# Performance work log

Hardware: AMD Instinct MI355X
Metric: run time of the kernel (lower is better)

The kernel has to match this reference:

```python
import jax, jax.numpy as jnp
import numpy as np
import math

T, N, F, A, NH = 2048, 64, 64, 64, 8
QG, QH, DG, DH = 256, 256, 256, 256
HORIZON = 16


def setup_inputs() -> dict:
    key = jax.random.key(0)
    ks = jax.random.split(key, 12)
    s = 0.05  # xavier-ish scale
    return {
        "x_fix": jax.random.normal(ks[0], (T, F), jnp.float32),
        "x_att": jax.random.normal(ks[1], (T, N, A), jnp.float32),
        "train_horizon": HORIZON,
        # query GRUCell: input = fix + 2*A*NH
        "q_gru_w_ih": jax.random.normal(ks[2], (3 * QG, F + 2 * A * NH), jnp.float32) * s,
        "q_gru_w_hh": jax.random.normal(ks[3], (3 * QG, QG), jnp.float32) * s,
        "q_gru_b_ih": jnp.zeros((3 * QG,), jnp.float32),
        "q_gru_b_hh": jnp.zeros((3 * QG,), jnp.float32),
        # q_hidden: input = QG + F + A*NH
        "q_hid_w": jax.random.normal(ks[4], (QH, QG + F + A * NH), jnp.float32) * s,
        "q_hid_b": jnp.zeros((QH,), jnp.float32),
        "weight_q": jax.random.normal(ks[5], (QH, A * NH), jnp.float32) * s,
        # decoder GRU: input = F + A*NH
        "dec_gru_w_ih": jax.random.normal(ks[6], (3 * DG, F + A * NH), jnp.float32) * s,
        "dec_gru_w_hh": jax.random.normal(ks[7], (3 * DG, DG), jnp.float32) * s,
        "dec_gru_b_ih": jnp.zeros((3 * DG,), jnp.float32),
        "dec_gru_b_hh": jnp.zeros((3 * DG,), jnp.float32),
        # dec_hidden: input = DG + F + A*NH + A
        "dec_hid_w": jax.random.normal(ks[8], (DH, DG + F + A * NH + A), jnp.float32) * s,
        "dec_hid_b": jnp.zeros((DH,), jnp.float32),
        "dec_out_w": jax.random.normal(ks[9], (A, DH), jnp.float32) * s,
        "dec_out_b": jnp.zeros((A,), jnp.float32),
    }


def _gru_cell(x, h, w_ih, w_hh, b_ih, b_hh):
    """PyTorch GRUCell math (gate order r,z,n)."""
    gi = w_ih @ x + b_ih
    gh = w_hh @ h + b_hh
    ir, iz, in_ = jnp.split(gi, 3)
    hr, hz, hn = jnp.split(gh, 3)
    r = jax.nn.sigmoid(ir + hr)
    z = jax.nn.sigmoid(iz + hz)
    n = jnp.tanh(in_ + r * hn)
    return (1.0 - z) * n + z * h


def reference(x_fix, x_att, train_horizon,
              q_gru_w_ih, q_gru_w_hh, q_gru_b_ih, q_gru_b_hh,
              q_hid_w, q_hid_b, weight_q,
              dec_gru_w_ih, dec_gru_w_hh, dec_gru_b_ih, dec_gru_b_hh,
              dec_hid_w, dec_hid_b, dec_out_w, dec_out_b):
    t, n_obj, a = x_att.shape
    nh_a = weight_q.shape[1]
    nh = nh_a // a
    scale = 1.0 / math.sqrt(a)

    # ---- recurrent query generation (sequential over time) ----
    def step(carry, inp):
        h, query = carry
        fix_t, att_t = inp                                   # [F], [N, A]
        attw = jax.nn.softmax((query.reshape(nh, a) @ att_t.T) * scale, axis=1)  # [NH, N]
        att_v = (attw @ att_t).reshape(-1)                   # [NH*A]
        h2 = _gru_cell(jnp.concatenate([fix_t, att_v, query]), h,
                       q_gru_w_ih, q_gru_w_hh, q_gru_b_ih, q_gru_b_hh)
        hid = jax.nn.relu(q_hid_w @ jnp.concatenate([h2, fix_t, att_v]) + q_hid_b)
        query2 = hid @ weight_q
        return (h2, query2), (attw, att_v)

    h0 = jnp.zeros((q_gru_w_hh.shape[1],), x_fix.dtype)
    q0 = jnp.ones((nh_a,), x_fix.dtype)
    (q_gru_n, query_n), (attw, att_a) = jax.lax.scan(step, (h0, q0), (x_fix, x_att))

    # ---- decoder (training path; dropout_p=0, noise_std=0 -> identity) ----
    hz = train_horizon
    # replicate-pad attw back hz steps in time, drop last hz: dec_attw[t] = attw[max(t-hz,0)]
    dec_attw = jnp.concatenate(
        [jnp.broadcast_to(attw[:1], (hz,) + attw.shape[1:]), attw[:-hz]], axis=0)  # [T, NH, N]
    dec_att_a = jnp.einsum('thn,tnd->thd', dec_attw, x_att).reshape(t, -1)          # [T, NH*A]
    dec_x = jnp.concatenate([x_fix, dec_att_a], axis=-1)                            # [T, F+NH*A]

    def dec_step(hd, xt):
        hd2 = _gru_cell(xt, hd, dec_gru_w_ih, dec_gru_w_hh, dec_gru_b_ih, dec_gru_b_hh)
        return hd2, hd2

    dg0 = jnp.zeros((dec_gru_w_hh.shape[1],), x_fix.dtype)
    dec_gru_n, dec_gru_a = jax.lax.scan(dec_step, dg0, dec_x)                       # [T, DG]

    feat = jnp.concatenate([dec_gru_a, dec_x], axis=-1)                             # [T, DG+F+NH*A]
    feat_b = jnp.broadcast_to(feat[:, None, :], (t, n_obj, feat.shape[-1]))
    inp = jnp.concatenate([feat_b, x_att], axis=-1)                                 # [T, N, DG+F+NH*A+A]
    hid = jax.nn.relu(inp @ dec_hid_w.T + dec_hid_b)
    pred = jax.nn.relu(hid @ dec_out_w.T + dec_out_b)                               # [T, N, A]

    return pred, attw, q_gru_n, dec_gru_n, query_n
```

## Files before the change

kernel.cpp:

```cpp
#include <hip/hip_runtime.h>
#include <math.h>

#define TT 2048
#define HZ 16
#define NBLK 32
#define NTH 512

#define OUT_ATTW   (2048*64*64)
#define OUT_QGRU   (OUT_ATTW + 2048*8*64)
#define OUT_DECGRU (OUT_QGRU + 256)
#define OUT_QN     (OUT_DECGRU + 256)

#define WSO_MB1    0
#define WSO_QACC   8192
#define WSO_QCNT   14336
#define WSO_ZEND   14464
#define WSO_GIFIX  14464
#define WSO_HIDFIX (WSO_GIFIX + 2048*768*4)
#define WSO_W2T    (WSO_HIDFIX + 2048*256*4)
#define WSO_DAVA   (WSO_W2T + 256*64*4)
#define WSO_DECH   (WSO_DAVA + 2048*512*4)
#define WSO_FEAT   (WSO_DECH + 2048*256*4)
#define WSO_SBUF   (WSO_FEAT + 2048*832*4)

__device__ __forceinline__ float warp_sum(float v) {
#pragma unroll
  for (int o = 32; o > 0; o >>= 1) v += __shfl_down(v, o, 64);
  return v;
}
__device__ __forceinline__ float warp_max(float v) {
#pragma unroll
  for (int o = 32; o > 0; o >>= 1) v = fmaxf(v, __shfl_down(v, o, 64));
  return v;
}
__device__ __forceinline__ float sigf(float x) { return 1.f / (1.f + __expf(-x)); }
__device__ __forceinline__ float dot4(float4 a, float4 b) {
  return a.x*b.x + a.y*b.y + a.z*b.z + a.w*b.w;
}
__device__ __forceinline__ unsigned long long aload64(const unsigned long long* p) {
  return __hip_atomic_load(p, __ATOMIC_RELAXED, __HIP_MEMORY_SCOPE_AGENT);
}
__device__ __forceinline__ void astore64(unsigned long long* p, unsigned long long v) {
  __hip_atomic_store(p, v, __ATOMIC_RELAXED, __HIP_MEMORY_SCOPE_AGENT);
}
__device__ __forceinline__ unsigned long long mbpack(float f, unsigned tag) {
  return ((unsigned long long)tag << 32) | (unsigned long long)__float_as_uint(f);
}
__device__ __forceinline__ float mbpoll(const unsigned long long* p, unsigned tag) {
  unsigned long long v = aload64(p);
  while ((unsigned)(v >> 32) != tag) {
    __builtin_amdgcn_s_sleep(1);
    v = aload64(p);
  }
  return __uint_as_float((unsigned)v);
}

__global__ void transpose_k(const float* __restrict__ w2,
                            float* __restrict__ w2T) {
  int e = blockIdx.x * 256 + threadIdx.x;
  int r = e >> 6, a = e & 63;
  w2T[e] = w2[a * 256 + r];
}

__global__ void __launch_bounds__(256) gemm64(
    const float* __restrict__ X, int ldx,
    const float* __restrict__ W, int ldw, int woff,
    const float* __restrict__ bias,
    float* __restrict__ C, int crows, int K) {
  __shared__ float Xs[64 * 65];
  __shared__ float Ws[64 * 65];
  int t0 = blockIdx.x * 64, r0 = blockIdx.y * 64;
  int tid = threadIdx.x;
  int u = tid & 15, v = tid >> 4;
  float acc[4][4];
#pragma unroll
  for (int i = 0; i < 4; i++)
#pragma unroll
    for (int j = 0; j < 4; j++) acc[i][j] = 0.f;

  for (int kc = 0; kc < K; kc += 64) {
    for (int idx = tid; idx < 4096; idx += 256) {
      int row = idx >> 6, col = idx & 63;
      Xs[row * 65 + col] = X[(size_t)(t0 + row) * ldx + kc + col];
      Ws[row * 65 + col] = W[(size_t)(r0 + row) * ldw + woff + kc + col];
    }
    __syncthreads();
#pragma unroll 8
    for (int k = 0; k < 64; k++) {
      float xs[4], ws[4];
#pragma unroll
      for (int i = 0; i < 4; i++) xs[i] = Xs[(v + 16 * i) * 65 + k];
#pragma unroll
      for (int j = 0; j < 4; j++) ws[j] = Ws[(u + 16 * j) * 65 + k];
#pragma unroll
      for (int i = 0; i < 4; i++)
#pragma unroll
        for (int j = 0; j < 4; j++) acc[i][j] += xs[i] * ws[j];
    }
    __syncthreads();
  }
#pragma unroll
  for (int i = 0; i < 4; i++)
#pragma unroll
    for (int j = 0; j < 4; j++) {
      int t = t0 + v + 16 * i, r = r0 + u + 16 * j;
      C[(size_t)t * crows + r] = acc[i][j] + bias[r];
    }
}

__global__ void __launch_bounds__(512) seq_kernel(
    const float* __restrict__ x_fix,
    const float* __restrict__ x_att,
    const float* __restrict__ w_ih,
    const float* __restrict__ w_hh,
    const float* __restrict__ b_hh,
    const float* __restrict__ q_hid_w,
    const float* __restrict__ wq,
    const float* __restrict__ dwih,
    const float* __restrict__ dwhh,
    const float* __restrict__ dbih,
    const float* __restrict__ dbhh,
    const float* __restrict__ gi_fix,
    const float* __restrict__ hid_fix,
    unsigned long long* __restrict__ mb1,
    float* __restrict__ qacc,
    unsigned* __restrict__ qcnt,
    float* __restrict__ dava,
    float* __restrict__ dec_hist,
    float* __restrict__ out) {
  __shared__ float att_s[64 * 65];
  __shared__ float ring_s[16][512];
  __shared__ __align__(16) float avq_s[1024];
  __shared__ float qk_s[512];
  __shared__ __align__(16) float xcat_s[576];
  __shared__ __align__(16) float hid8_s[8];
  __shared__ __align__(16) float h_s[256];
  __shared__ __align__(16) float dech_s[256];
  __shared__ float g_s[4][8];
  __shared__ float dg_s[4][8];

  const int tid = threadIdx.x;
  const int bid = blockIdx.x;
  const int lane = tid & 63, wv = tid >> 6;

  for (int i = tid; i < 1024; i += NTH) avq_s[i] = (i >= 512) ? 1.f : 0.f;
  if (tid < 256) { h_s[tid] = 0.f; dech_s[tid] = 0.f; }
  {
    const float4* g4 = (const float4*)x_att;
    float4 a = g4[tid * 2], b = g4[tid * 2 + 1];
    int row = tid >> 3, c0 = (tid & 7) * 8;
    float* d = &att_s[row * 65 + c0];
    d[0]=a.x; d[1]=a.y; d[2]=a.z; d[3]=a.w; d[4]=b.x; d[5]=b.y; d[6]=b.z; d[7]=b.w;
  }
  if (tid < 64) xcat_s[tid] = x_fix[tid];
  __syncthreads();

  for (int t = 0; t <= TT; ++t) {
    if (t > 0) {
      {
        float f = mbpoll(mb1 + (size_t)((t - 1) & 1) * 512 + tid, (unsigned)t);
        int b = tid >> 4, j = tid & 15;
        if (j < 8) h_s[b * 8 + j] = f;
        else dech_s[b * 8 + j - 8] = f;
        if (t >= 2 && tid < 16)
          __hip_atomic_store(&qacc[(size_t)((t - 1) % 3) * 512 + bid * 16 + tid],
                             0.f, __ATOMIC_RELAXED, __HIP_MEMORY_SCOPE_AGENT);
      }
      __syncthreads();
      {
        int row = bid * 8 + wv;
        const float4* W = (const float4*)(q_hid_w + (size_t)row * 832);
        float acc = dot4(W[lane], ((const float4*)h_s)[lane]);
        acc += dot4(W[80 + lane], ((const float4*)avq_s)[lane]);
        acc += dot4(W[144 + lane], ((const float4*)avq_s)[64 + lane]);
        float s = warp_sum(acc);
        if (lane == 0)
          hid8_s[wv] = fmaxf(s + hid_fix[(size_t)(t - 1) * 256 + row], 0.f);
      }
      __syncthreads();
      {
        float hv[8];
#pragma unroll
        for (int r = 0; r < 8; r++) hv[r] = hid8_s[r];
        float partial = 0.f;
#pragma unroll
        for (int r = 0; r < 8; r++)
          partial += hv[r] * wq[(size_t)(bid * 8 + r) * 512 + tid];
        __hip_atomic_fetch_add(&qacc[(size_t)(t % 3) * 512 + tid], partial,
                               __ATOMIC_RELAXED, __HIP_MEMORY_SCOPE_AGENT);
        asm volatile("s_waitcnt vmcnt(0)" ::: "memory");
      }
      __syncthreads();
      if (tid == 0) {
        __hip_atomic_fetch_add(qcnt, 1u, __ATOMIC_RELAXED,
                               __HIP_MEMORY_SCOPE_AGENT);
        unsigned target = 32u * (unsigned)t;
        while (__hip_atomic_load(qcnt, __ATOMIC_RELAXED,
                                 __HIP_MEMORY_SCOPE_AGENT) < target)
          __builtin_amdgcn_s_sleep(1);
      }
      __syncthreads();
      {
        float qv = __hip_atomic_load(&qacc[(size_t)(t % 3) * 512 + tid],
                                     __ATOMIC_RELAXED, __HIP_MEMORY_SCOPE_AGENT);
        avq_s[512 + tid] = qv;
        if (t == TT) {
          if (bid == 0) {
            if (tid < 256) {
              out[OUT_QGRU + tid] = h_s[tid];
              out[OUT_DECGRU + tid] = dech_s[tid];
            }
            out[OUT_QN + tid] = qv;
          }
          break;
        }
      }
      __syncthreads();
    }

    float4 pfa, pfb;
    {
      int tn = (t + 1 < TT) ? t + 1 : t;
      const float4* g4 = (const float4*)(x_att + (size_t)tn * 4096);
      pfa = g4[tid * 2];
      pfb = g4[tid * 2 + 1];
    }
    {
      float acc = 0.f;
#pragma unroll 16
      for (int a = 0; a < 64; a++)
        acc += avq_s[512 + wv * 64 + a] * att_s[lane * 65 + a];
      acc *= 0.125f;
      float m = __shfl(warp_max(acc), 0, 64);
      float e = __expf(acc - m);
      float s = __shfl(warp_sum(e), 0, 64);
      qk_s[wv * 64 + lane] = e / s;
    }
    {
      const float* rg = (t == 0) ? &qk_s[0] : ring_s[(t >= 16) ? (t & 15) : 0];
      float av = 0.f, dv = 0.f;
#pragma unroll 8
      for (int n = 0; n < 64; n++) {
        float xv = att_s[n * 65 + lane];
        av += qk_s[wv * 64 + n] * xv;
        dv += rg[wv * 64 + n] * xv;
      }
      avq_s[wv * 64 + lane] = av;
      xcat_s[64 + wv * 64 + lane] = dv;
    }
    __syncthreads();
    {
      float accg[3], acch[3];
      int rows[3];
#pragma unroll
      for (int k = 0; k < 3; k++) {
        int m = wv * 3 + k;
        rows[k] = ((m >> 3) * 256) + bid * 8 + (m & 7);
        accg[k] = 0.f; acch[k] = 0.f;
      }
      const float4* in4 = (const float4*)avq_s;
#pragma unroll
      for (int c0 = 0; c0 < 4; c0++) {
        int c = lane + 64 * c0;
        float4 v = in4[c];
#pragma unroll
        for (int k = 0; k < 3; k++) {
          const float4* W = (const float4*)(w_ih + (size_t)rows[k] * 1088 + 64);
          accg[k] += dot4(W[c], v);
        }
      }
      {
        const float4* h4 = (const float4*)h_s;
        float4 vh = h4[lane];
#pragma unroll
        for (int k = 0; k < 3; k++) {
          const float4* Wh = (const float4*)(w_hh + (size_t)rows[k] * 256);
          acch[k] += dot4(Wh[lane], vh);
        }
      }
#pragma unroll
      for (int k = 0; k < 3; k++) {
        int m = wv * 3 + k;
        int gate = m >> 3, idx = m & 7;
        if (gate < 2) {
          float s = warp_sum(accg[k] + acch[k]);
          if (lane == 0)
            g_s[gate][idx] = s + gi_fix[(size_t)t * 768 + rows[k]] + b_hh[rows[k]];
        } else {
          float sg = warp_sum(accg[k]);
          float sh = warp_sum(acch[k]);
          if (lane == 0) {
            g_s[2][idx] = sg + gi_fix[(size_t)t * 768 + rows[k]];
            g_s[3][idx] = sh + b_hh[rows[k]];
          }
        }
      }
    }
    {
      float accg[3], acch[3];
      int rows[3];
#pragma unroll
      for (int k = 0; k < 3; k++) {
        int m = wv * 3 + k;
        rows[k] = ((m >> 3) * 256) + bid * 8 + (m & 7);
        accg[k] = 0.f; acch[k] = 0.f;
      }
      const float4* x4 = (const float4*)xcat_s;
#pragma unroll
      for (int c0 = 0; c0 < 3; c0++) {
        int c = lane + 64 * c0;
        if (c < 144) {
          float4 v = x4[c];
#pragma unroll
          for (int k = 0; k < 3; k++) {
            const float4* W = (const float4*)(dwih + (size_t)rows[k] * 576);
            accg[k] += dot4(W[c], v);
          }
        }
      }
      {
        const float4* dh4 = (const float4*)dech_s;
        float4 vh = dh4[lane];
#pragma unroll
        for (int k = 0; k < 3; k++) {
          const float4* Wh = (const float4*)(dwhh + (size_t)rows[k] * 256);
          acch[k] += dot4(Wh[lane], vh);
        }
      }
#pragma unroll
      for (int k = 0; k < 3; k++) {
        int m = wv * 3 + k;
        int gate = m >> 3, idx = m & 7;
        if (gate < 2) {
          float s = warp_sum(accg[k] + acch[k]);
          if (lane == 0)
            dg_s[gate][idx] = s + dbih[rows[k]] + dbhh[rows[k]];
        } else {
          float sg = warp_sum(accg[k]);
          float sh = warp_sum(acch[k]);
          if (lane == 0) {
            dg_s[2][idx] = sg + dbih[rows[k]];
            dg_s[3][idx] = sh + dbhh[rows[k]];
          }
        }
      }
    }
    __syncthreads();
    if (tid < 8) {
      float r = sigf(g_s[0][tid]), z = sigf(g_s[1][tid]);
      float nn = tanhf(g_s[2][tid] + r * g_s[3][tid]);
      float h2 = (1.f - z) * nn + z * h_s[bid * 8 + tid];
      astore64(&mb1[(size_t)(t & 1) * 512 + bid * 16 + tid],
               mbpack(h2, (unsigned)(t + 1)));
    } else if (tid < 16) {
      int i = tid - 8;
      float r = sigf(dg_s[0][i]), z = sigf(dg_s[1][i]);
      float nn = tanhf(dg_s[2][i] + r * dg_s[3][i]);
      float d2 = (1.f - z) * nn + z * dech_s[bid * 8 + i];
      astore64(&mb1[(size_t)(t & 1) * 512 + bid * 16 + tid],
               mbpack(d2, (unsigned)(t + 1)));
      dec_hist[(size_t)t * 256 + bid * 8 + i] = d2;
    }
    if (tid < 16) {
      out[OUT_ATTW + (size_t)t * 512 + bid * 16 + tid] = qk_s[bid * 16 + tid];
      dava[(size_t)t * 512 + bid * 16 + tid] = xcat_s[64 + bid * 16 + tid];
    }
    ring_s[t & 15][tid] = qk_s[tid];
    {
      int row = tid >> 3, c0 = (tid & 7) * 8;
      float* d = &att_s[row * 65 + c0];
      d[0]=pfa.x; d[1]=pfa.y; d[2]=pfa.z; d[3]=pfa.w;
      d[4]=pfb.x; d[5]=pfb.y; d[6]=pfb.z; d[7]=pfb.w;
    }
    if (tid >= 448) {
      int i = tid - 448;
      int tn = (t + 1 < TT) ? t + 1 : t;
      xcat_s[i] = x_fix[tn * 64 + i];
    }
  }
}

__global__ void featcopy(const float* __restrict__ dec_hist,
                         const float* __restrict__ x_fix,
                         const float* __restrict__ dava,
                         float* __restrict__ feat) {
  int t = blockIdx.x, tid = threadIdx.x;
  float* f = feat + (size_t)t * 832;
  f[tid] = dec_hist[(size_t)t * 256 + tid];
  if (tid < 64) f[256 + tid] = x_fix[t * 64 + tid];
  for (int i = tid; i < 512; i += 256) f[320 + i] = dava[(size_t)t * 512 + i];
}

__global__ void __launch_bounds__(256) final_k(
    const float* __restrict__ x_att,
    const float* __restrict__ s,
    const float* __restrict__ w1,
    const float* __restrict__ w2T,
    const float* __restrict__ b2,
    float* __restrict__ pred) {
  __shared__ float att_s[4096];
  __shared__ float s_s[256];
  __shared__ float hid_s[32 * 256];
  int t = blockIdx.x, tid = threadIdx.x, lane = tid & 63, wv = tid >> 6;
  for (int i = tid; i < 4096; i += 256) att_s[i] = x_att[(size_t)t * 4096 + i];
  s_s[tid] = s[(size_t)t * 256 + tid];
  float4 w1v[16];
  const float4* W1a4 = (const float4*)(w1 + (size_t)tid * 896 + 832);
#pragma unroll
  for (int q = 0; q < 16; q++) w1v[q] = W1a4[q];
  float bb = b2[lane];
  __syncthreads();
  for (int ch = 0; ch < 2; ch++) {
    for (int nl = 0; nl < 32; nl++) {
      int n = ch * 32 + nl;
      const float4* a4 = (const float4*)(att_s + n * 64);
      float acc = s_s[tid];
#pragma unroll
      for (int q = 0; q < 16; q++) acc += dot4(w1v[q], a4[q]);
      hid_s[nl * 256 + tid] = fmaxf(acc, 0.f);
    }
    __syncthreads();
    float accb[8];
#pragma unroll
    for (int j = 0; j < 8; j++) accb[j] = bb;
    for (int r = 0; r < 256; r++) {
      float w = w2T[r * 64 + lane];
#pragma unroll
      for (int j = 0; j < 8; j++) accb[j] += w * hid_s[(wv * 8 + j) * 256 + r];
    }
#pragma unroll
    for (int j = 0; j < 8; j++) {
      int n = ch * 32 + wv * 8 + j;
      pred[(size_t)t * 4096 + n * 64 + lane] = fmaxf(accb[j], 0.f);
    }
    __syncthreads();
  }
}

extern "C" void kernel_launch(void* const* d_in, const int* in_sizes, int n_in,
                              void* d_out, int out_size, void* d_ws, size_t ws_size,
                              hipStream_t stream) {
  const float* x_fix = (const float*)d_in[0];
  const float* x_att = (const float*)d_in[1];
  const float* qwih = (const float*)d_in[3];
  const float* qwhh = (const float*)d_in[4];
  const float* qbih = (const float*)d_in[5];
  const float* qbhh = (const float*)d_in[6];
  const float* qhw = (const float*)d_in[7];
  const float* qhb = (const float*)d_in[8];
  const float* wq = (const float*)d_in[9];
  const float* dwih = (const float*)d_in[10];
  const float* dwhh = (const float*)d_in[11];
  const float* dbih = (const float*)d_in[12];
  const float* dbhh = (const float*)d_in[13];
  const float* w1 = (const float*)d_in[14];
  const float* b1 = (const float*)d_in[15];
  const float* w2 = (const float*)d_in[16];
  const float* b2 = (const float*)d_in[17];
  float* out = (float*)d_out;

  char* ws = (char*)d_ws;
  unsigned long long* mb1 = (unsigned long long*)(ws + WSO_MB1);
  float* qacc = (float*)(ws + WSO_QACC);
  unsigned* qcnt = (unsigned*)(ws + WSO_QCNT);
  float* gi_fix = (float*)(ws + WSO_GIFIX);
  float* hid_fix = (float*)(ws + WSO_HIDFIX);
  float* w2T = (float*)(ws + WSO_W2T);
  float* dava = (float*)(ws + WSO_DAVA);
  float* dec_hist = (float*)(ws + WSO_DECH);
  float* feat = (float*)(ws + WSO_FEAT);
  float* sbuf = (float*)(ws + WSO_SBUF);

  hipMemsetAsync(ws, 0, WSO_ZEND, stream);

  transpose_k<<<64, 256, 0, stream>>>(w2, w2T);
  gemm64<<<dim3(32, 12), 256, 0, stream>>>(x_fix, 64, qwih, 1088, 0, qbih,
                                           gi_fix, 768, 64);
  gemm64<<<dim3(32, 4), 256, 0, stream>>>(x_fix, 64, qhw, 832, 256, qhb,
                                          hid_fix, 256, 64);

  seq_kernel<<<NBLK, NTH, 0, stream>>>(x_fix, x_att, qwih, qwhh, qbhh,
                                       qhw, wq, dwih, dwhh, dbih, dbhh,
                                       gi_fix, hid_fix, mb1, qacc, qcnt,
                                       dava, dec_hist, out);

  featcopy<<<2048, 256, 0, stream>>>(dec_hist, x_fix, dava, feat);
  gemm64<<<dim3(32, 4), 256, 0, stream>>>(feat, 832, w1, 896, 0, b1,
                                          sbuf, 256, 832);
  final_k<<<2048, 256, 0, stream>>>(x_att, sbuf, w1, w2T, b2, out);
}
```

Measured before the change: 22.72 ms.

## Restructure sequential loop with fixed-point atomic reductions and counter-tagged completion polling

Reorganises the per-timestep cross-block schedule of the persistent recurrent kernel. The q_hidden projection becomes a scatter-reduce over a transposed weight, using fixed-point 64-bit atomics whose top byte counts contributions, so consumers poll for completion instead of sharing a global counter barrier. The hidden-state matvecs and the decoder GRU input are moved after the mailbox exchange so they overlap with waiting, and ring-buffer slots are cleared for reuse. The aim is fewer grid-wide synchronisation round trips per step, at the cost of fixed-point precision loss and more complex slot-recycling logic.

```diff
diff --git a/kernel.cpp b/kernel.cpp
--- a/kernel.cpp
+++ b/kernel.cpp
@@ -2,7 +2,6 @@
 #include <math.h>
 
 #define TT 2048
-#define HZ 16
 #define NBLK 32
 #define NTH 512
 
@@ -12,16 +11,19 @@
 #define OUT_QN     (OUT_DECGRU + 256)
 
 #define WSO_MB1    0
-#define WSO_QACC   8192
-#define WSO_QCNT   14336
-#define WSO_ZEND   14464
-#define WSO_GIFIX  14464
+#define WSO_HIDACC 8192
+#define WSO_QACC   16384
+#define WSO_ZEND   32768
+#define WSO_GIFIX  32768
 #define WSO_HIDFIX (WSO_GIFIX + 2048*768*4)
-#define WSO_W2T    (WSO_HIDFIX + 2048*256*4)
+#define WSO_QHWT   (WSO_HIDFIX + 2048*256*4)
+#define WSO_W2T    (WSO_QHWT + 832*256*4)
 #define WSO_DAVA   (WSO_W2T + 256*64*4)
 #define WSO_DECH   (WSO_DAVA + 2048*512*4)
 #define WSO_FEAT   (WSO_DECH + 2048*256*4)
 #define WSO_SBUF   (WSO_FEAT + 2048*832*4)
+
+#define PAYMASK ((1ULL<<56)-1)
 
 __device__ __forceinline__ float warp_sum(float v) {
 #pragma unroll
@@ -54,12 +56,41 @@
   }
   return __uint_as_float((unsigned)v);
 }
-
-__global__ void transpose_k(const float* __restrict__ w2,
+__device__ __forceinline__ unsigned long long rpack(float v) {
+  long long f = (long long)((double)v * 268435456.0);
+  return (1ULL << 56) + (unsigned long long)(f + (1LL << 41));
+}
+__device__ __forceinline__ float runpack(unsigned long long u) {
+  long long S = (long long)(u & PAYMASK) - (32LL << 41);
+  return (float)((double)S * 3.725290298461914e-09);
+}
+__device__ __forceinline__ unsigned long long cpoll(unsigned long long* p) {
+  unsigned long long u = aload64(p);
+  while ((u >> 56) != 32ULL) {
+    __builtin_amdgcn_s_sleep(1);
+    u = aload64(p);
+  }
+  return u;
+}
+__device__ __forceinline__ void radd(unsigned long long* p, float v) {
+  __hip_atomic_fetch_add(p, rpack(v), __ATOMIC_RELAXED, __HIP_MEMORY_SCOPE_AGENT);
+}
+
+__global__ void transpose_k(const float* __restrict__ qhw,
+                            const float* __restrict__ w2,
+                            float* __restrict__ qhwT,
                             float* __restrict__ w2T) {
-  int e = blockIdx.x * 256 + threadIdx.x;
-  int r = e >> 6, a = e & 63;
-  w2T[e] = w2[a * 256 + r];
+  int g = blockIdx.x * 256 + threadIdx.x;
+  if (g < 832 * 256) {
+    int c = g >> 8, r = g & 255;
+    qhwT[g] = qhw[r * 832 + c];
+  } else {
+    int e = g - 832 * 256;
+    if (e < 16384) {
+      int r = e >> 6, a = e & 63;
+      w2T[e] = w2[a * 256 + r];
+    }
+  }
 }
 
 __global__ void __launch_bounds__(256) gemm64(
@@ -114,7 +145,7 @@
     const float* __restrict__ w_ih,
     const float* __restrict__ w_hh,
     const float* __restrict__ b_hh,
-    const float* __restrict__ q_hid_w,
+    const float* __restrict__ qhwT,
     const float* __restrict__ wq,
     const float* __restrict__ dwih,
     const float* __restrict__ dwhh,
@@ -123,8 +154,8 @@
     const float* __restrict__ gi_fix,
     const float* __restrict__ hid_fix,
     unsigned long long* __restrict__ mb1,
-    float* __restrict__ qacc,
-    unsigned* __restrict__ qcnt,
+    unsigned long long* __restrict__ hidacc,
+    unsigned long long* __restrict__ qacc,
     float* __restrict__ dava,
     float* __restrict__ dec_hist,
     float* __restrict__ out) {
@@ -133,7 +164,8 @@
   __shared__ __align__(16) float avq_s[1024];
   __shared__ float qk_s[512];
   __shared__ __align__(16) float xcat_s[576];
-  __shared__ __align__(16) float hid8_s[8];
+  __shared__ float hidown_s[8];
+  __shared__ float h2own_s[8];
   __shared__ __align__(16) float h_s[256];
   __shared__ __align__(16) float dech_s[256];
   __shared__ float g_s[4][8];
@@ -142,6 +174,14 @@
   const int tid = threadIdx.x;
   const int bid = blockIdx.x;
   const int lane = tid & 63, wv = tid >> 6;
+
+  int qrows[3];
+#pragma unroll
+  for (int k = 0; k < 3; k++) {
+    int m = wv * 3 + k;
+    qrows[k] = ((m >> 3) * 256) + bid * 8 + (m & 7);
+  }
+  float acch_q[3] = {0.f, 0.f, 0.f};
 
   for (int i = tid; i < 1024; i += NTH) avq_s[i] = (i >= 512) ? 1.f : 0.f;
   if (tid < 256) { h_s[tid] = 0.f; dech_s[tid] = 0.f; }
@@ -155,75 +195,17 @@
   if (tid < 64) xcat_s[tid] = x_fix[tid];
   __syncthreads();
 
-  for (int t = 0; t <= TT; ++t) {
-    if (t > 0) {
-      {
-        float f = mbpoll(mb1 + (size_t)((t - 1) & 1) * 512 + tid, (unsigned)t);
-        int b = tid >> 4, j = tid & 15;
-        if (j < 8) h_s[b * 8 + j] = f;
-        else dech_s[b * 8 + j - 8] = f;
-        if (t >= 2 && tid < 16)
-          __hip_atomic_store(&qacc[(size_t)((t - 1) % 3) * 512 + bid * 16 + tid],
-                             0.f, __ATOMIC_RELAXED, __HIP_MEMORY_SCOPE_AGENT);
-      }
-      __syncthreads();
-      {
-        int row = bid * 8 + wv;
-        const float4* W = (const float4*)(q_hid_w + (size_t)row * 832);
-        float acc = dot4(W[lane], ((const float4*)h_s)[lane]);
-        acc += dot4(W[80 + lane], ((const float4*)avq_s)[lane]);
-        acc += dot4(W[144 + lane], ((const float4*)avq_s)[64 + lane]);
-        float s = warp_sum(acc);
-        if (lane == 0)
-          hid8_s[wv] = fmaxf(s + hid_fix[(size_t)(t - 1) * 256 + row], 0.f);
-      }
-      __syncthreads();
-      {
-        float hv[8];
-#pragma unroll
-        for (int r = 0; r < 8; r++) hv[r] = hid8_s[r];
-        float partial = 0.f;
-#pragma unroll
-        for (int r = 0; r < 8; r++)
-          partial += hv[r] * wq[(size_t)(bid * 8 + r) * 512 + tid];
-        __hip_atomic_fetch_add(&qacc[(size_t)(t % 3) * 512 + tid], partial,
-                               __ATOMIC_RELAXED, __HIP_MEMORY_SCOPE_AGENT);
-        asm volatile("s_waitcnt vmcnt(0)" ::: "memory");
-      }
-      __syncthreads();
-      if (tid == 0) {
-        __hip_atomic_fetch_add(qcnt, 1u, __ATOMIC_RELAXED,
-                               __HIP_MEMORY_SCOPE_AGENT);
-        unsigned target = 32u * (unsigned)t;
-        while (__hip_atomic_load(qcnt, __ATOMIC_RELAXED,
-                                 __HIP_MEMORY_SCOPE_AGENT) < target)
-          __builtin_amdgcn_s_sleep(1);
-      }
-      __syncthreads();
-      {
-        float qv = __hip_atomic_load(&qacc[(size_t)(t % 3) * 512 + tid],
-                                     __ATOMIC_RELAXED, __HIP_MEMORY_SCOPE_AGENT);
-        avq_s[512 + tid] = qv;
-        if (t == TT) {
-          if (bid == 0) {
-            if (tid < 256) {
-              out[OUT_QGRU + tid] = h_s[tid];
-              out[OUT_DECGRU + tid] = dech_s[tid];
-            }
-            out[OUT_QN + tid] = qv;
-          }
-          break;
-        }
-      }
-      __syncthreads();
-    }
-
+  for (int t = 0; t < TT; ++t) {
+    const int HB = t & 3;
+    const int QB = (t + 1) & 3;
     float4 pfa, pfb;
+    float fixpf = 0.f;
     {
       int tn = (t + 1 < TT) ? t + 1 : t;
       const float4* g4 = (const float4*)(x_att + (size_t)tn * 4096);
       pfa = g4[tid * 2];
       pfb = g4[tid * 2 + 1];
+      if (tid >= 448) fixpf = x_fix[tn * 64 + (tid - 448)];
     }
     {
       float acc = 0.f;
@@ -236,28 +218,17 @@
       float s = __shfl(warp_sum(e), 0, 64);
       qk_s[wv * 64 + lane] = e / s;
     }
-    {
-      const float* rg = (t == 0) ? &qk_s[0] : ring_s[(t >= 16) ? (t & 15) : 0];
-      float av = 0.f, dv = 0.f;
+    __syncthreads();
+    {
+      float av = 0.f;
 #pragma unroll 8
-      for (int n = 0; n < 64; n++) {
-        float xv = att_s[n * 65 + lane];
-        av += qk_s[wv * 64 + n] * xv;
-        dv += rg[wv * 64 + n] * xv;
-      }
+      for (int n = 0; n < 64; n++) av += qk_s[wv * 64 + n] * att_s[n * 65 + lane];
       avq_s[wv * 64 + lane] = av;
-      xcat_s[64 + wv * 64 + lane] = dv;
-    }
-    __syncthreads();
-    {
-      float accg[3], acch[3];
-      int rows[3];
-#pragma unroll
-      for (int k = 0; k < 3; k++) {
-        int m = wv * 3 + k;
-        rows[k] = ((m >> 3) * 256) + bid * 8 + (m & 7);
-        accg[k] = 0.f; acch[k] = 0.f;
-      }
+      if (t == 0) xcat_s[64 + wv * 64 + lane] = av;
+    }
+    __syncthreads();
+    {
+      float accg[3] = {0.f, 0.f, 0.f};
       const float4* in4 = (const float4*)avq_s;
 #pragma unroll
       for (int c0 = 0; c0 < 4; c0++) {
@@ -265,17 +236,8 @@
         float4 v = in4[c];
 #pragma unroll
         for (int k = 0; k < 3; k++) {
-          const float4* W = (const float4*)(w_ih + (size_t)rows[k] * 1088 + 64);
+          const float4* W = (const float4*)(w_ih + (size_t)qrows[k] * 1088 + 64);
           accg[k] += dot4(W[c], v);
-        }
-      }
-      {
-        const float4* h4 = (const float4*)h_s;
-        float4 vh = h4[lane];
-#pragma unroll
-        for (int k = 0; k < 3; k++) {
-          const float4* Wh = (const float4*)(w_hh + (size_t)rows[k] * 256);
-          acch[k] += dot4(Wh[lane], vh);
         }
       }
 #pragma unroll
@@ -283,28 +245,21 @@
         int m = wv * 3 + k;
         int gate = m >> 3, idx = m & 7;
         if (gate < 2) {
-          float s = warp_sum(accg[k] + acch[k]);
+          float s = warp_sum(accg[k] + acch_q[k]);
           if (lane == 0)
-            g_s[gate][idx] = s + gi_fix[(size_t)t * 768 + rows[k]] + b_hh[rows[k]];
+            g_s[gate][idx] = s + gi_fix[(size_t)t * 768 + qrows[k]] + b_hh[qrows[k]];
         } else {
           float sg = warp_sum(accg[k]);
-          float sh = warp_sum(acch[k]);
+          float sh = warp_sum(acch_q[k]);
           if (lane == 0) {
-            g_s[2][idx] = sg + gi_fix[(size_t)t * 768 + rows[k]];
-            g_s[3][idx] = sh + b_hh[rows[k]];
+            g_s[2][idx] = sg + gi_fix[(size_t)t * 768 + qrows[k]];
+            g_s[3][idx] = sh + b_hh[qrows[k]];
           }
         }
       }
     }
-    {
-      float accg[3], acch[3];
-      int rows[3];
-#pragma unroll
-      for (int k = 0; k < 3; k++) {
-        int m = wv * 3 + k;
-        rows[k] = ((m >> 3) * 256) + bid * 8 + (m & 7);
-        accg[k] = 0.f; acch[k] = 0.f;
-      }
+    if (t == 0) {
+      float accg[3] = {0.f, 0.f, 0.f};
       const float4* x4 = (const float4*)xcat_s;
 #pragma unroll
       for (int c0 = 0; c0 < 3; c0++) {
@@ -313,18 +268,9 @@
           float4 v = x4[c];
 #pragma unroll
           for (int k = 0; k < 3; k++) {
-            const float4* W = (const float4*)(dwih + (size_t)rows[k] * 576);
+            const float4* W = (const float4*)(dwih + (size_t)qrows[k] * 576);
             accg[k] += dot4(W[c], v);
           }
-        }
-      }
-      {
-        const float4* dh4 = (const float4*)dech_s;
-        float4 vh = dh4[lane];
-#pragma unroll
-        for (int k = 0; k < 3; k++) {
-          const float4* Wh = (const float4*)(dwhh + (size_t)rows[k] * 256);
-          acch[k] += dot4(Wh[lane], vh);
         }
       }
 #pragma unroll
@@ -332,15 +278,13 @@
         int m = wv * 3 + k;
         int gate = m >> 3, idx = m & 7;
         if (gate < 2) {
-          float s = warp_sum(accg[k] + acch[k]);
-          if (lane == 0)
-            dg_s[gate][idx] = s + dbih[rows[k]] + dbhh[rows[k]];
+          float s = warp_sum(accg[k]);
+          if (lane == 0) dg_s[gate][idx] = s + dbih[qrows[k]] + dbhh[qrows[k]];
         } else {
           float sg = warp_sum(accg[k]);
-          float sh = warp_sum(acch[k]);
           if (lane == 0) {
-            dg_s[2][idx] = sg + dbih[rows[k]];
-            dg_s[3][idx] = sh + dbhh[rows[k]];
+            dg_s[2][idx] = sg + dbih[qrows[k]];
+            dg_s[3][idx] = dbhh[qrows[k]];
           }
         }
       }
@@ -350,6 +294,7 @@
       float r = sigf(g_s[0][tid]), z = sigf(g_s[1][tid]);
       float nn = tanhf(g_s[2][tid] + r * g_s[3][tid]);
       float h2 = (1.f - z) * nn + z * h_s[bid * 8 + tid];
+      h2own_s[tid] = h2;
       astore64(&mb1[(size_t)(t & 1) * 512 + bid * 16 + tid],
                mbpack(h2, (unsigned)(t + 1)));
     } else if (tid < 16) {
@@ -360,10 +305,12 @@
       astore64(&mb1[(size_t)(t & 1) * 512 + bid * 16 + tid],
                mbpack(d2, (unsigned)(t + 1)));
       dec_hist[(size_t)t * 256 + bid * 8 + i] = d2;
-    }
-    if (tid < 16) {
-      out[OUT_ATTW + (size_t)t * 512 + bid * 16 + tid] = qk_s[bid * 16 + tid];
-      dava[(size_t)t * 512 + bid * 16 + tid] = xcat_s[64 + bid * 16 + tid];
+    } else if (tid < 32) {
+      int i = tid - 16;
+      out[OUT_ATTW + (size_t)t * 512 + bid * 16 + i] = qk_s[bid * 16 + i];
+    } else if (tid < 48) {
+      int i = tid - 32;
+      dava[(size_t)t * 512 + bid * 16 + i] = xcat_s[64 + bid * 16 + i];
     }
     ring_s[t & 15][tid] = qk_s[tid];
     {
@@ -372,11 +319,118 @@
       d[0]=pfa.x; d[1]=pfa.y; d[2]=pfa.z; d[3]=pfa.w;
       d[4]=pfb.x; d[5]=pfb.y; d[6]=pfb.z; d[7]=pfb.w;
     }
-    if (tid >= 448) {
-      int i = tid - 448;
-      int tn = (t + 1 < TT) ? t + 1 : t;
-      xcat_s[i] = x_fix[tn * 64 + i];
-    }
+    __syncthreads();
+    if (tid < 256) {
+      float c = 0.f;
+      const float* Wh = qhwT + (size_t)(bid * 8) * 256 + tid;
+#pragma unroll
+      for (int k = 0; k < 8; k++) c += Wh[k * 256] * h2own_s[k];
+      const float* Wa = qhwT + (size_t)(320 + bid * 16) * 256 + tid;
+#pragma unroll
+      for (int k = 0; k < 16; k++) c += Wa[k * 256] * avq_s[bid * 16 + k];
+      radd(&hidacc[(size_t)HB * 256 + tid], c);
+    }
+    if (t >= 1) astore64(&qacc[(size_t)((t - 1) & 3) * 512 + tid], 0ULL);
+    if (tid < 8) {
+      unsigned long long* slot = &hidacc[(size_t)HB * 256 + bid * 8 + tid];
+      unsigned long long u = cpoll(slot);
+      astore64(slot, 0ULL);
+      hidown_s[tid] =
+          fmaxf(runpack(u) + hid_fix[(size_t)t * 256 + bid * 8 + tid], 0.f);
+    } else {
+      int jj = tid - 8;
+      int slot_t1 = (t + 1 >= 16) ? ((t + 1) & 15) : 0;
+      const float* rg = ring_s[slot_t1];
+      {
+        int h = jj >> 6, a = jj & 63;
+        float dv = 0.f;
+#pragma unroll 8
+        for (int n = 0; n < 64; n++) dv += rg[h * 64 + n] * att_s[n * 65 + a];
+        xcat_s[64 + jj] = dv;
+      }
+      if (jj < 8) {
+        int j2 = jj + 504, h = j2 >> 6, a = j2 & 63;
+        float dv = 0.f;
+#pragma unroll 8
+        for (int n = 0; n < 64; n++) dv += rg[h * 64 + n] * att_s[n * 65 + a];
+        xcat_s[64 + j2] = dv;
+      }
+      if (tid >= 448) xcat_s[tid - 448] = fixpf;
+    }
+    __syncthreads();
+    {
+      float p = 0.f;
+#pragma unroll
+      for (int k = 0; k < 8; k++)
+        p += hidown_s[k] * wq[(size_t)(bid * 8 + k) * 512 + tid];
+      radd(&qacc[(size_t)QB * 512 + tid], p);
+    }
+    {
+      float f = mbpoll(mb1 + (size_t)(t & 1) * 512 + tid, (unsigned)(t + 1));
+      int b = tid >> 4, j = tid & 15;
+      if (j < 8) h_s[b * 8 + j] = f;
+      else dech_s[b * 8 + j - 8] = f;
+    }
+    __syncthreads();
+    {
+      const float4* h4 = (const float4*)h_s;
+      float4 vh = h4[lane];
+#pragma unroll
+      for (int k = 0; k < 3; k++) {
+        const float4* Wh = (const float4*)(w_hh + (size_t)qrows[k] * 256);
+        acch_q[k] = dot4(Wh[lane], vh);
+      }
+      float accg[3] = {0.f, 0.f, 0.f}, acch[3];
+      const float4* x4 = (const float4*)xcat_s;
+#pragma unroll
+      for (int c0 = 0; c0 < 3; c0++) {
+        int c = lane + 64 * c0;
+        if (c < 144) {
+          float4 v = x4[c];
+#pragma unroll
+          for (int k = 0; k < 3; k++) {
+            const float4* W = (const float4*)(dwih + (size_t)qrows[k] * 576);
+            accg[k] += dot4(W[c], v);
+          }
+        }
+      }
+      const float4* dh4 = (const float4*)dech_s;
+      float4 vd = dh4[lane];
+#pragma unroll
+      for (int k = 0; k < 3; k++) {
+        const float4* Wh = (const float4*)(dwhh + (size_t)qrows[k] * 256);
+        acch[k] = dot4(Wh[lane], vd);
+      }
+#pragma unroll
+      for (int k = 0; k < 3; k++) {
+        int m = wv * 3 + k;
+        int gate = m >> 3, idx = m & 7;
+        if (gate < 2) {
+          float s = warp_sum(accg[k] + acch[k]);
+          if (lane == 0) dg_s[gate][idx] = s + dbih[qrows[k]] + dbhh[qrows[k]];
+        } else {
+          float sg = warp_sum(accg[k]);
+          float sh = warp_sum(acch[k]);
+          if (lane == 0) {
+            dg_s[2][idx] = sg + dbih[qrows[k]];
+            dg_s[3][idx] = sh + dbhh[qrows[k]];
+          }
+        }
+      }
+    }
+    {
+      unsigned long long u = cpoll(&qacc[(size_t)QB * 512 + tid]);
+      avq_s[512 + tid] = runpack(u);
+    }
+    __syncthreads();
+  }
+
+  if (bid == 0) {
+    if (tid < 256) {
+      out[OUT_QGRU + tid] = h_s[tid];
+      out[OUT_DECGRU + tid] = dech_s[tid];
+    }
+    out[OUT_QN + tid] = avq_s[512 + tid];
   }
 }
 
@@ -461,10 +515,11 @@
 
   char* ws = (char*)d_ws;
   unsigned long long* mb1 = (unsigned long long*)(ws + WSO_MB1);
-  float* qacc = (float*)(ws + WSO_QACC);
-  unsigned* qcnt = (unsigned*)(ws + WSO_QCNT);
+  unsigned long long* hidacc = (unsigned long long*)(ws + WSO_HIDACC);
+  unsigned long long* qacc = (unsigned long long*)(ws + WSO_QACC);
   float* gi_fix = (float*)(ws + WSO_GIFIX);
   float* hid_fix = (float*)(ws + WSO_HIDFIX);
+  float* qhwT = (float*)(ws + WSO_QHWT);
   float* w2T = (float*)(ws + WSO_W2T);
   float* dava = (float*)(ws + WSO_DAVA);
   float* dec_hist = (float*)(ws + WSO_DECH);
@@ -473,15 +528,15 @@
 
   hipMemsetAsync(ws, 0, WSO_ZEND, stream);
 
-  transpose_k<<<64, 256, 0, stream>>>(w2, w2T);
+  transpose_k<<<896, 256, 0, stream>>>(qhw, w2, qhwT, w2T);
   gemm64<<<dim3(32, 12), 256, 0, stream>>>(x_fix, 64, qwih, 1088, 0, qbih,
                                            gi_fix, 768, 64);
   gemm64<<<dim3(32, 4), 256, 0, stream>>>(x_fix, 64, qhw, 832, 256, qhb,
                                           hid_fix, 256, 64);
 
   seq_kernel<<<NBLK, NTH, 0, stream>>>(x_fix, x_att, qwih, qwhh, qbhh,
-                                       qhw, wq, dwih, dwhh, dbih, dbhh,
-                                       gi_fix, hid_fix, mb1, qacc, qcnt,
+                                       qhwT, wq, dwih, dwhh, dbih, dbhh,
+                                       gi_fix, hid_fix, mb1, hidacc, qacc,
                                        dava, dec_hist, out);
 
   featcopy<<<2048, 256, 0, stream>>>(dec_hist, x_fix, dava, feat);
```

Result: slower. 29.75 ms (+30.9%).
